# Kernel optimization log

Hardware: AMD Instinct MI355X
Metric: run time of the kernel (lower is better)

Reference implementation:

```python
import jax, jax.numpy as jnp
import numpy as np

D = 1024
P = 10  # log2(D)
N = 16384


def _fft_idx(p, j):
    perm = np.arange(2 ** p)
    _mask = 2 ** (j + 1) - 1
    __mask = 2 ** j - 1
    mask_ = ~_mask
    perm_ = perm & mask_
    _perm = perm & _mask
    __perm = perm & __mask
    idx_uv = (__perm << 1) + (_perm >> j) + perm_
    idx_x = perm ^ 2 ** j
    return idx_uv, idx_x

# Static (P, D) permutation tables, computed once at import time.
_IDX_UV = np.stack([_fft_idx(P, j)[0] for j in range(P)])  # permutes UV vectors
_IDX_X = np.stack([_fft_idx(P, j)[1] for j in range(P)])   # permutes the input per stage
IDX_UV = jnp.asarray(_IDX_UV)


def _interleave(a, b):
    # a, b: (P, D//2) -> (P, D) with a at even slots, b at odd slots
    return jnp.stack([a, b], axis=-1).reshape(a.shape[0], -1)


def _uv_fft(theta, phi):
    # Deterministic UV_FFT (sigma_BS = 0, new=False path)
    s1 = jnp.sin(theta / 2)
    c1 = jnp.cos(theta / 2)
    s2 = jnp.sin(theta / 2 + phi)
    c2 = jnp.cos(theta / 2 + phi)
    u_re = _interleave(-s1 * s2, s1 ** 2)
    v_re = _interleave(-c1 * s1, -c1 * s2)
    u_im = _interleave(s1 * c2, -c1 * s1)
    v_im = _interleave(c1 ** 2, c1 * c2)
    # per-layer permutation of the UV vectors
    u_re = jnp.take_along_axis(u_re, IDX_UV, axis=1)
    v_re = jnp.take_along_axis(v_re, IDX_UV, axis=1)
    u_im = jnp.take_along_axis(u_im, IDX_UV, axis=1)
    v_im = jnp.take_along_axis(v_im, IDX_UV, axis=1)
    return u_re, v_re, u_im, v_im


def setup_inputs() -> dict:
    key = jax.random.key(0)
    k1, k2, k3, k4 = jax.random.split(key, 4)
    X = jax.random.normal(k1, (N, 2 * D), dtype=jnp.float32)
    theta = jnp.arcsin(jax.random.uniform(k2, (P, D // 2), dtype=jnp.float32))
    phi = jax.random.uniform(k3, (P, D // 2), dtype=jnp.float32) * (2 * np.pi)
    psi = jax.random.uniform(k4, (D,), dtype=jnp.float32) * (2 * np.pi)
    return {"X": X, "theta": theta, "phi": phi, "psi": psi}


def reference(X, theta, phi, psi):
    u_re, v_re, u_im, v_im = _uv_fft(theta, phi)
    Xr = X[:, :D]
    Xi = X[:, D:]
    # P = log2(D) sequential butterfly stages (small static unrolled loop)
    for j in range(P):
        perm = _IDX_X[j]  # static numpy index -> compiled gather
        sr = Xr[:, perm]
        si = Xi[:, perm]
        Yr = u_re[j] * Xr - u_im[j] * Xi + (v_re[j] * sr - v_im[j] * si)
        Yi = u_re[j] * Xi + u_im[j] * Xr + (v_re[j] * si + v_im[j] * sr)
        Xr, Xi = Yr, Yi
    # final diagonal phase layer (use_psi=True)
    cp = jnp.cos(psi)
    sp = jnp.sin(psi)
    Yr = cp * Xr - sp * Xi
    Yi = cp * Xi + sp * Xr
    return jnp.concatenate([Yr, Yi], axis=1)
```

## Files before the change

kernel.cpp:

```cpp
#include <hip/hip_runtime.h>

#define P 10
#define D 1024
#define NROWS 16384

typedef float nfloat4 __attribute__((ext_vector_type(4)));

__global__ void coef_kernel(const float* __restrict__ theta,
                            const float* __restrict__ phi,
                            const float* __restrict__ psi,
                            float4* __restrict__ coef) {
    int idx = blockIdx.x * blockDim.x + threadIdx.x;
    if (idx >= P * D) return;
    int j = idx >> 10;
    int slot = idx & (D - 1);
    int e = slot >> 6;
    int lane = slot & 63;
    int k = ((e >> 2) << 8) + (lane << 2) + (e & 3);
    int b = (k >> j) & 1;
    unsigned lowmask = (1u << j) - 1u;
    unsigned m = ((unsigned)k & lowmask) | (((unsigned)k >> 1) & ~lowmask);
    float th = theta[j * (D / 2) + m];
    float ph = phi[j * (D / 2) + m];
    float h = th * 0.5f;
    float s1 = sinf(h), c1 = cosf(h);
    float s2 = sinf(h + ph), c2 = cosf(h + ph);
    float ur, ui, vr, vi;
    if (b) { ur =  s1 * s1; vr = -c1 * s2; ui = -c1 * s1; vi = c1 * c2; }
    else   { ur = -s1 * s2; vr = -c1 * s1; ui =  s1 * c2; vi = c1 * c1; }
    if (j == P - 1) {
        float ps = psi[k];
        float cp = cosf(ps), sp = sinf(ps);
        float ur2 = cp * ur - sp * ui, ui2 = sp * ur + cp * ui;
        float vr2 = cp * vr - sp * vi, vi2 = sp * vr + cp * vi;
        ur = ur2; ui = ui2; vr = vr2; vi = vi2;
    }
    coef[idx] = make_float4(ur, ui, vr, vi);
}

template <int J, int PM>
__device__ __forceinline__ void stage_intra(float (&ra)[16], float (&ia)[16],
                                            float (&rb)[16], float (&ib)[16],
                                            const float4* __restrict__ coef, int lane) {
    const float4* cj = coef + J * D + lane;
#pragma unroll
    for (int e0 = 0; e0 < 16; ++e0) {
        if (e0 & PM) continue;
        const int e1 = e0 | PM;
        float4 c0 = cj[e0 * 64];
        float4 c1 = cj[e1 * 64];
        float ar0 = ra[e0], ai0 = ia[e0], ar1 = ra[e1], ai1 = ia[e1];
        float br0 = rb[e0], bi0 = ib[e0], br1 = rb[e1], bi1 = ib[e1];
        ra[e0] = c0.x * ar0 - c0.y * ai0 + c0.z * ar1 - c0.w * ai1;
        ia[e0] = c0.x * ai0 + c0.y * ar0 + c0.z * ai1 + c0.w * ar1;
        ra[e1] = c1.x * ar1 - c1.y * ai1 + c1.z * ar0 - c1.w * ai0;
        ia[e1] = c1.x * ai1 + c1.y * ar1 + c1.z * ai0 + c1.w * ar0;
        rb[e0] = c0.x * br0 - c0.y * bi0 + c0.z * br1 - c0.w * bi1;
        ib[e0] = c0.x * bi0 + c0.y * br0 + c0.z * bi1 + c0.w * br1;
        rb[e1] = c1.x * br1 - c1.y * bi1 + c1.z * br0 - c1.w * bi0;
        ib[e1] = c1.x * bi1 + c1.y * br1 + c1.z * bi0 + c1.w * br0;
    }
}

template <int J>
__device__ __forceinline__ void stage_shfl(float (&ra)[16], float (&ia)[16],
                                           float (&rb)[16], float (&ib)[16],
                                           const float4* __restrict__ coef, int lane) {
    const int mask = 1 << (J - 2);
    const float4* cj = coef + J * D + lane;
#pragma unroll
    for (int e = 0; e < 16; ++e) {
        float4 c = cj[e * 64];
        float sra = __shfl_xor(ra[e], mask);
        float sia = __shfl_xor(ia[e], mask);
        float srb = __shfl_xor(rb[e], mask);
        float sib = __shfl_xor(ib[e], mask);
        float nra = c.x * ra[e] - c.y * ia[e] + c.z * sra - c.w * sia;
        float nia = c.x * ia[e] + c.y * ra[e] + c.z * sia + c.w * sra;
        float nrb = c.x * rb[e] - c.y * ib[e] + c.z * srb - c.w * sib;
        float nib = c.x * ib[e] + c.y * rb[e] + c.z * sib + c.w * srb;
        ra[e] = nra; ia[e] = nia; rb[e] = nrb; ib[e] = nib;
    }
}

__global__ __launch_bounds__(256) void fft_kernel(const float* __restrict__ X,
                                                  const float4* __restrict__ coef,
                                                  float* __restrict__ out) {
    const int lane = threadIdx.x & 63;
    const int wave = threadIdx.x >> 6;
    const long rowbase = (long)blockIdx.x * 8 + (long)wave * 2;
    const float* x0 = X + rowbase * 2048 + lane * 4;
    const float* x1 = x0 + 2048;

    float ra[16], ia[16], rb[16], ib[16];
#pragma unroll
    for (int eh = 0; eh < 4; ++eh) {
        float4 v0r = *(const float4*)(x0 + eh * 256);
        float4 v0i = *(const float4*)(x0 + 1024 + eh * 256);
        float4 v1r = *(const float4*)(x1 + eh * 256);
        float4 v1i = *(const float4*)(x1 + 1024 + eh * 256);
        ra[eh * 4 + 0] = v0r.x; ra[eh * 4 + 1] = v0r.y; ra[eh * 4 + 2] = v0r.z; ra[eh * 4 + 3] = v0r.w;
        ia[eh * 4 + 0] = v0i.x; ia[eh * 4 + 1] = v0i.y; ia[eh * 4 + 2] = v0i.z; ia[eh * 4 + 3] = v0i.w;
        rb[eh * 4 + 0] = v1r.x; rb[eh * 4 + 1] = v1r.y; rb[eh * 4 + 2] = v1r.z; rb[eh * 4 + 3] = v1r.w;
        ib[eh * 4 + 0] = v1i.x; ib[eh * 4 + 1] = v1i.y; ib[eh * 4 + 2] = v1i.z; ib[eh * 4 + 3] = v1i.w;
    }

    stage_intra<0, 1>(ra, ia, rb, ib, coef, lane);
    stage_intra<1, 2>(ra, ia, rb, ib, coef, lane);

    stage_shfl<2>(ra, ia, rb, ib, coef, lane);
    stage_shfl<3>(ra, ia, rb, ib, coef, lane);
    stage_shfl<4>(ra, ia, rb, ib, coef, lane);
    stage_shfl<5>(ra, ia, rb, ib, coef, lane);
    stage_shfl<6>(ra, ia, rb, ib, coef, lane);
    stage_shfl<7>(ra, ia, rb, ib, coef, lane);

    stage_intra<8, 4>(ra, ia, rb, ib, coef, lane);
    stage_intra<9, 8>(ra, ia, rb, ib, coef, lane);

    float* o0 = out + rowbase * 2048 + lane * 4;
    float* o1 = o0 + 2048;
#pragma unroll
    for (int eh = 0; eh < 4; ++eh) {
        nfloat4 v0r = { ra[eh * 4 + 0], ra[eh * 4 + 1], ra[eh * 4 + 2], ra[eh * 4 + 3] };
        nfloat4 v0i = { ia[eh * 4 + 0], ia[eh * 4 + 1], ia[eh * 4 + 2], ia[eh * 4 + 3] };
        nfloat4 v1r = { rb[eh * 4 + 0], rb[eh * 4 + 1], rb[eh * 4 + 2], rb[eh * 4 + 3] };
        nfloat4 v1i = { ib[eh * 4 + 0], ib[eh * 4 + 1], ib[eh * 4 + 2], ib[eh * 4 + 3] };
        __builtin_nontemporal_store(v0r, (nfloat4*)(o0 + eh * 256));
        __builtin_nontemporal_store(v0i, (nfloat4*)(o0 + 1024 + eh * 256));
        __builtin_nontemporal_store(v1r, (nfloat4*)(o1 + eh * 256));
        __builtin_nontemporal_store(v1i, (nfloat4*)(o1 + 1024 + eh * 256));
    }
}

extern "C" void kernel_launch(void* const* d_in, const int* in_sizes, int n_in,
                              void* d_out, int out_size, void* d_ws, size_t ws_size,
                              hipStream_t stream) {
    const float* X     = (const float*)d_in[0];
    const float* theta = (const float*)d_in[1];
    const float* phi   = (const float*)d_in[2];
    const float* psi   = (const float*)d_in[3];
    float4* coef = (float4*)d_ws;

    coef_kernel<<<(P * D + 255) / 256, 256, 0, stream>>>(theta, phi, psi, coef);
    fft_kernel<<<NROWS / 8, 256, 0, stream>>>(X, coef, (float*)d_out);
}
```

Baseline: 77.50 us.

## Stage butterfly coefficients through double-buffered LDS shared across block waves

Each block now cooperatively loads each stage's coefficient table from global memory into a double-buffered shared-memory array and prefetches the next stage's coefficients into registers while the current stage computes. All four waves read coefficients from LDS instead of each issuing its own global/L2 loads. This adds a block-wide barrier per stage, 32 KB of LDS per block that may limit occupancy, and extra register pressure for the staged prefetch.

```diff
diff --git a/kernel.cpp b/kernel.cpp
--- a/kernel.cpp
+++ b/kernel.cpp
@@ -38,17 +38,16 @@
     coef[idx] = make_float4(ur, ui, vr, vi);
 }
 
-template <int J, int PM>
+template <int PM>
 __device__ __forceinline__ void stage_intra(float (&ra)[16], float (&ia)[16],
                                             float (&rb)[16], float (&ib)[16],
-                                            const float4* __restrict__ coef, int lane) {
-    const float4* cj = coef + J * D + lane;
+                                            const float4* lsrc, int lane) {
 #pragma unroll
     for (int e0 = 0; e0 < 16; ++e0) {
         if (e0 & PM) continue;
         const int e1 = e0 | PM;
-        float4 c0 = cj[e0 * 64];
-        float4 c1 = cj[e1 * 64];
+        float4 c0 = lsrc[e0 * 64 + lane];
+        float4 c1 = lsrc[e1 * 64 + lane];
         float ar0 = ra[e0], ai0 = ia[e0], ar1 = ra[e1], ai1 = ia[e1];
         float br0 = rb[e0], bi0 = ib[e0], br1 = rb[e1], bi1 = ib[e1];
         ra[e0] = c0.x * ar0 - c0.y * ai0 + c0.z * ar1 - c0.w * ai1;
@@ -62,19 +61,17 @@
     }
 }
 
-template <int J>
+template <int MASK>
 __device__ __forceinline__ void stage_shfl(float (&ra)[16], float (&ia)[16],
                                            float (&rb)[16], float (&ib)[16],
-                                           const float4* __restrict__ coef, int lane) {
-    const int mask = 1 << (J - 2);
-    const float4* cj = coef + J * D + lane;
+                                           const float4* lsrc, int lane) {
 #pragma unroll
     for (int e = 0; e < 16; ++e) {
-        float4 c = cj[e * 64];
-        float sra = __shfl_xor(ra[e], mask);
-        float sia = __shfl_xor(ia[e], mask);
-        float srb = __shfl_xor(rb[e], mask);
-        float sib = __shfl_xor(ib[e], mask);
+        float4 c = lsrc[e * 64 + lane];
+        float sra = __shfl_xor(ra[e], MASK);
+        float sia = __shfl_xor(ia[e], MASK);
+        float srb = __shfl_xor(rb[e], MASK);
+        float sib = __shfl_xor(ib[e], MASK);
         float nra = c.x * ra[e] - c.y * ia[e] + c.z * sra - c.w * sia;
         float nia = c.x * ia[e] + c.y * ra[e] + c.z * sia + c.w * sra;
         float nrb = c.x * rb[e] - c.y * ib[e] + c.z * srb - c.w * sib;
@@ -83,11 +80,25 @@
     }
 }
 
+__device__ __forceinline__ void pre_load(const float4* __restrict__ coef, int j,
+                                         int tid, float4 (&st)[4]) {
+#pragma unroll
+    for (int i = 0; i < 4; ++i) st[i] = coef[j * D + i * 256 + tid];
+}
+
+__device__ __forceinline__ void commit(float4* dst, int tid, const float4 (&st)[4]) {
+#pragma unroll
+    for (int i = 0; i < 4; ++i) dst[i * 256 + tid] = st[i];
+    __syncthreads();
+}
+
 __global__ __launch_bounds__(256) void fft_kernel(const float* __restrict__ X,
                                                   const float4* __restrict__ coef,
                                                   float* __restrict__ out) {
-    const int lane = threadIdx.x & 63;
-    const int wave = threadIdx.x >> 6;
+    __shared__ float4 lc[2][D];
+    const int tid  = threadIdx.x;
+    const int lane = tid & 63;
+    const int wave = tid >> 6;
     const long rowbase = (long)blockIdx.x * 8 + (long)wave * 2;
     const float* x0 = X + rowbase * 2048 + lane * 4;
     const float* x1 = x0 + 2048;
@@ -105,18 +116,18 @@
         ib[eh * 4 + 0] = v1i.x; ib[eh * 4 + 1] = v1i.y; ib[eh * 4 + 2] = v1i.z; ib[eh * 4 + 3] = v1i.w;
     }
 
-    stage_intra<0, 1>(ra, ia, rb, ib, coef, lane);
-    stage_intra<1, 2>(ra, ia, rb, ib, coef, lane);
-
-    stage_shfl<2>(ra, ia, rb, ib, coef, lane);
-    stage_shfl<3>(ra, ia, rb, ib, coef, lane);
-    stage_shfl<4>(ra, ia, rb, ib, coef, lane);
-    stage_shfl<5>(ra, ia, rb, ib, coef, lane);
-    stage_shfl<6>(ra, ia, rb, ib, coef, lane);
-    stage_shfl<7>(ra, ia, rb, ib, coef, lane);
-
-    stage_intra<8, 4>(ra, ia, rb, ib, coef, lane);
-    stage_intra<9, 8>(ra, ia, rb, ib, coef, lane);
+    float4 st[4];
+    pre_load(coef, 0, tid, st); commit(&lc[0][0], tid, st);
+    pre_load(coef, 1, tid, st); stage_intra<1>(ra, ia, rb, ib, &lc[0][0], lane); commit(&lc[1][0], tid, st);
+    pre_load(coef, 2, tid, st); stage_intra<2>(ra, ia, rb, ib, &lc[1][0], lane); commit(&lc[0][0], tid, st);
+    pre_load(coef, 3, tid, st); stage_shfl<1>(ra, ia, rb, ib, &lc[0][0], lane);  commit(&lc[1][0], tid, st);
+    pre_load(coef, 4, tid, st); stage_shfl<2>(ra, ia, rb, ib, &lc[1][0], lane);  commit(&lc[0][0], tid, st);
+    pre_load(coef, 5, tid, st); stage_shfl<4>(ra, ia, rb, ib, &lc[0][0], lane);  commit(&lc[1][0], tid, st);
+    pre_load(coef, 6, tid, st); stage_shfl<8>(ra, ia, rb, ib, &lc[1][0], lane);  commit(&lc[0][0], tid, st);
+    pre_load(coef, 7, tid, st); stage_shfl<16>(ra, ia, rb, ib, &lc[0][0], lane); commit(&lc[1][0], tid, st);
+    pre_load(coef, 8, tid, st); stage_shfl<32>(ra, ia, rb, ib, &lc[1][0], lane); commit(&lc[0][0], tid, st);
+    pre_load(coef, 9, tid, st); stage_intra<4>(ra, ia, rb, ib, &lc[0][0], lane); commit(&lc[1][0], tid, st);
+    stage_intra<8>(ra, ia, rb, ib, &lc[1][0], lane);
 
     float* o0 = out + rowbase * 2048 + lane * 4;
     float* o1 = o0 + 2048;
```

Measured after the change: 106.4 us. 37.2% more time.

## Store compact per-pair sin/cos table and factor butterfly math for stages 0-8

Applied to the files above, without the earlier changes.

Replaces the per-element (ur,ui,vr,vi) table for stages 0-8 with a per-butterfly-pair (s1,c1,s2,c2) table, halving the coefficient bytes those stages read. The intra-thread stages apply a factored 2x2 rotation built from these values, and the shuffle stages rebuild the coefficients per lane from the side bit. Stage 9 keeps the full table with psi folded in. Coefficient memory traffic drops, at the cost of a few extra multiplies and selects per element, in a kernel that is likely bound by streaming X.

```diff
diff --git a/kernel.cpp b/kernel.cpp
--- a/kernel.cpp
+++ b/kernel.cpp
@@ -9,44 +9,122 @@
 __global__ void coef_kernel(const float* __restrict__ theta,
                             const float* __restrict__ phi,
                             const float* __restrict__ psi,
-                            float4* __restrict__ coef) {
+                            float4* __restrict__ ctab) {
     int idx = blockIdx.x * blockDim.x + threadIdx.x;
-    if (idx >= P * D) return;
-    int j = idx >> 10;
-    int slot = idx & (D - 1);
-    int e = slot >> 6;
-    int lane = slot & 63;
-    int k = ((e >> 2) << 8) + (lane << 2) + (e & 3);
-    int b = (k >> j) & 1;
-    unsigned lowmask = (1u << j) - 1u;
-    unsigned m = ((unsigned)k & lowmask) | (((unsigned)k >> 1) & ~lowmask);
-    float th = theta[j * (D / 2) + m];
-    float ph = phi[j * (D / 2) + m];
-    float h = th * 0.5f;
-    float s1 = sinf(h), c1 = cosf(h);
-    float s2 = sinf(h + ph), c2 = cosf(h + ph);
-    float ur, ui, vr, vi;
-    if (b) { ur =  s1 * s1; vr = -c1 * s2; ui = -c1 * s1; vi = c1 * c2; }
-    else   { ur = -s1 * s2; vr = -c1 * s1; ui =  s1 * c2; vi = c1 * c1; }
-    if (j == P - 1) {
+    if (idx >= 9 * 512 + 1024) return;
+    if (idx < 9 * 512) {
+        int j = idx >> 9;
+        int slot = idx & 511;
+        int k0;
+        if (j < 2 || j == 8) {
+            int PM = (j == 0) ? 1 : (j == 1) ? 2 : 4;
+            int pidx = slot >> 6, lane = slot & 63;
+            int e0 = (pidx & (PM - 1)) | ((pidx & ~(PM - 1)) << 1);
+            k0 = ((e0 >> 2) << 8) | (lane << 2) | (e0 & 3);
+        } else {
+            int mask = 1 << (j - 2);
+            int e = slot >> 5, lanec = slot & 31;
+            int lane0 = (lanec & (mask - 1)) | ((lanec & ~(mask - 1)) << 1);
+            k0 = ((e >> 2) << 8) | (lane0 << 2) | (e & 3);
+        }
+        unsigned lowmask = (1u << j) - 1u;
+        unsigned m = ((unsigned)k0 & lowmask) | (((unsigned)k0 >> 1) & ~lowmask);
+        float th = theta[j * (D / 2) + m];
+        float ph = phi[j * (D / 2) + m];
+        float h = th * 0.5f;
+        ctab[idx] = make_float4(sinf(h), cosf(h), sinf(h + ph), cosf(h + ph));
+    } else {
+        int s = idx - 9 * 512;
+        int e = s >> 6, lane = s & 63;
+        int k = ((e >> 2) << 8) | (lane << 2) | (e & 3);
+        int b = (k >> 9) & 1;
+        unsigned m = (unsigned)k & 511u;
+        float th = theta[9 * (D / 2) + m];
+        float ph = phi[9 * (D / 2) + m];
+        float h = th * 0.5f;
+        float s1 = sinf(h), c1 = cosf(h);
+        float s2 = sinf(h + ph), c2 = cosf(h + ph);
+        float ur, ui, vr, vi;
+        if (b) { ur =  s1 * s1; vr = -c1 * s2; ui = -c1 * s1; vi = c1 * c2; }
+        else   { ur = -s1 * s2; vr = -c1 * s1; ui =  s1 * c2; vi = c1 * c1; }
         float ps = psi[k];
         float cp = cosf(ps), sp = sinf(ps);
         float ur2 = cp * ur - sp * ui, ui2 = sp * ur + cp * ui;
         float vr2 = cp * vr - sp * vi, vi2 = sp * vr + cp * vi;
-        ur = ur2; ui = ui2; vr = vr2; vi = vi2;
-    }
-    coef[idx] = make_float4(ur, ui, vr, vi);
+        ctab[5120 + s] = make_float4(ur2, ui2, vr2, vi2);
+    }
 }
 
 template <int J, int PM>
-__device__ __forceinline__ void stage_intra(float (&ra)[16], float (&ia)[16],
-                                            float (&rb)[16], float (&ib)[16],
-                                            const float4* __restrict__ coef, int lane) {
-    const float4* cj = coef + J * D + lane;
+__device__ __forceinline__ void stage_intra_c(float (&ra)[16], float (&ia)[16],
+                                              float (&rb)[16], float (&ib)[16],
+                                              const float4* __restrict__ ctab, int lane) {
+    const float4* cj = ctab + J * 512 + lane;
 #pragma unroll
     for (int e0 = 0; e0 < 16; ++e0) {
         if (e0 & PM) continue;
         const int e1 = e0 | PM;
+        const int pidx = (e0 & (PM - 1)) | ((e0 >> 1) & ~(PM - 1));
+        float4 c = cj[pidx * 64];
+        float s1 = c.x, c1 = c.y, s2 = c.z, c2 = c.w;
+        {
+            float Pr = s2 * ra[e0] + c2 * ia[e0];
+            float Pi = c2 * ra[e0] - s2 * ia[e0];
+            float Qr = s1 * ra[e1] + c1 * ia[e1];
+            float Qi = c1 * ra[e1] - s1 * ia[e1];
+            ra[e0] = -(s1 * Pr + c1 * Qr);
+            ia[e0] =   s1 * Pi + c1 * Qi;
+            ra[e1] =   s1 * Qr - c1 * Pr;
+            ia[e1] =   c1 * Pi - s1 * Qi;
+        }
+        {
+            float Pr = s2 * rb[e0] + c2 * ib[e0];
+            float Pi = c2 * rb[e0] - s2 * ib[e0];
+            float Qr = s1 * rb[e1] + c1 * ib[e1];
+            float Qi = c1 * rb[e1] - s1 * ib[e1];
+            rb[e0] = -(s1 * Pr + c1 * Qr);
+            ib[e0] =   s1 * Pi + c1 * Qi;
+            rb[e1] =   s1 * Qr - c1 * Pr;
+            ib[e1] =   c1 * Pi - s1 * Qi;
+        }
+    }
+}
+
+template <int J>
+__device__ __forceinline__ void stage_shfl_c(float (&ra)[16], float (&ia)[16],
+                                             float (&rb)[16], float (&ib)[16],
+                                             const float4* __restrict__ ctab, int lane) {
+    const int mask = 1 << (J - 2);
+    const int lanec = (lane & (mask - 1)) | ((lane >> 1) & ~(mask - 1));
+    const bool bs = (lane & mask) != 0;
+    const float4* cj = ctab + J * 512 + lanec;
+#pragma unroll
+    for (int e = 0; e < 16; ++e) {
+        float4 c = cj[e * 32];
+        float s1 = c.x, c1 = c.y, s2 = c.z, c2 = c.w;
+        float ur =  s1 * (bs ?  s1 : -s2);
+        float ui =  s1 * (bs ? -c1 :  c2);
+        float vr = -c1 * (bs ?  s2 :  s1);
+        float vi =  c1 * (bs ?  c2 :  c1);
+        float sra = __shfl_xor(ra[e], mask);
+        float sia = __shfl_xor(ia[e], mask);
+        float srb = __shfl_xor(rb[e], mask);
+        float sib = __shfl_xor(ib[e], mask);
+        float nra = ur * ra[e] - ui * ia[e] + vr * sra - vi * sia;
+        float nia = ur * ia[e] + ui * ra[e] + vr * sia + vi * sra;
+        float nrb = ur * rb[e] - ui * ib[e] + vr * srb - vi * sib;
+        float nib = ur * ib[e] + ui * rb[e] + vr * sib + vi * srb;
+        ra[e] = nra; ia[e] = nia; rb[e] = nrb; ib[e] = nib;
+    }
+}
+
+__device__ __forceinline__ void stage9(float (&ra)[16], float (&ia)[16],
+                                       float (&rb)[16], float (&ib)[16],
+                                       const float4* __restrict__ c9, int lane) {
+    const float4* cj = c9 + lane;
+#pragma unroll
+    for (int e0 = 0; e0 < 8; ++e0) {
+        const int e1 = e0 | 8;
         float4 c0 = cj[e0 * 64];
         float4 c1 = cj[e1 * 64];
         float ar0 = ra[e0], ai0 = ia[e0], ar1 = ra[e1], ai1 = ia[e1];
@@ -62,29 +140,8 @@
     }
 }
 
-template <int J>
-__device__ __forceinline__ void stage_shfl(float (&ra)[16], float (&ia)[16],
-                                           float (&rb)[16], float (&ib)[16],
-                                           const float4* __restrict__ coef, int lane) {
-    const int mask = 1 << (J - 2);
-    const float4* cj = coef + J * D + lane;
-#pragma unroll
-    for (int e = 0; e < 16; ++e) {
-        float4 c = cj[e * 64];
-        float sra = __shfl_xor(ra[e], mask);
-        float sia = __shfl_xor(ia[e], mask);
-        float srb = __shfl_xor(rb[e], mask);
-        float sib = __shfl_xor(ib[e], mask);
-        float nra = c.x * ra[e] - c.y * ia[e] + c.z * sra - c.w * sia;
-        float nia = c.x * ia[e] + c.y * ra[e] + c.z * sia + c.w * sra;
-        float nrb = c.x * rb[e] - c.y * ib[e] + c.z * srb - c.w * sib;
-        float nib = c.x * ib[e] + c.y * rb[e] + c.z * sib + c.w * srb;
-        ra[e] = nra; ia[e] = nia; rb[e] = nrb; ib[e] = nib;
-    }
-}
-
 __global__ __launch_bounds__(256) void fft_kernel(const float* __restrict__ X,
-                                                  const float4* __restrict__ coef,
+                                                  const float4* __restrict__ ctab,
                                                   float* __restrict__ out) {
     const int lane = threadIdx.x & 63;
     const int wave = threadIdx.x >> 6;
@@ -105,18 +162,18 @@
         ib[eh * 4 + 0] = v1i.x; ib[eh * 4 + 1] = v1i.y; ib[eh * 4 + 2] = v1i.z; ib[eh * 4 + 3] = v1i.w;
     }
 
-    stage_intra<0, 1>(ra, ia, rb, ib, coef, lane);
-    stage_intra<1, 2>(ra, ia, rb, ib, coef, lane);
-
-    stage_shfl<2>(ra, ia, rb, ib, coef, lane);
-    stage_shfl<3>(ra, ia, rb, ib, coef, lane);
-    stage_shfl<4>(ra, ia, rb, ib, coef, lane);
-    stage_shfl<5>(ra, ia, rb, ib, coef, lane);
-    stage_shfl<6>(ra, ia, rb, ib, coef, lane);
-    stage_shfl<7>(ra, ia, rb, ib, coef, lane);
-
-    stage_intra<8, 4>(ra, ia, rb, ib, coef, lane);
-    stage_intra<9, 8>(ra, ia, rb, ib, coef, lane);
+    stage_intra_c<0, 1>(ra, ia, rb, ib, ctab, lane);
+    stage_intra_c<1, 2>(ra, ia, rb, ib, ctab, lane);
+
+    stage_shfl_c<2>(ra, ia, rb, ib, ctab, lane);
+    stage_shfl_c<3>(ra, ia, rb, ib, ctab, lane);
+    stage_shfl_c<4>(ra, ia, rb, ib, ctab, lane);
+    stage_shfl_c<5>(ra, ia, rb, ib, ctab, lane);
+    stage_shfl_c<6>(ra, ia, rb, ib, ctab, lane);
+    stage_shfl_c<7>(ra, ia, rb, ib, ctab, lane);
+
+    stage_intra_c<8, 4>(ra, ia, rb, ib, ctab, lane);
+    stage9(ra, ia, rb, ib, ctab + 5120, lane);
 
     float* o0 = out + rowbase * 2048 + lane * 4;
     float* o1 = o0 + 2048;
@@ -140,8 +197,8 @@
     const float* theta = (const float*)d_in[1];
     const float* phi   = (const float*)d_in[2];
     const float* psi   = (const float*)d_in[3];
-    float4* coef = (float4*)d_ws;
-
-    coef_kernel<<<(P * D + 255) / 256, 256, 0, stream>>>(theta, phi, psi, coef);
-    fft_kernel<<<NROWS / 8, 256, 0, stream>>>(X, coef, (float*)d_out);
-}
+    float4* ctab = (float4*)d_ws;
+
+    coef_kernel<<<(9 * 512 + 1024 + 255) / 256, 256, 0, stream>>>(theta, phi, psi, ctab);
+    fft_kernel<<<NROWS / 8, 256, 0, stream>>>(X, ctab, (float*)d_out);
+}
```

Measured after the change: 139.6 us. 80.1% more time.
